# Optimization experiments

Hardware: AMD Instinct MI355X
Metric: run time of the kernel (lower is better)

The kernel has to match this reference:

```python
import jax, jax.numpy as jnp
import numpy as np
from math import sqrt


def setup_inputs() -> dict:
    key = jax.random.key(0)
    kq, kk, kv = jax.random.split(key, 3)
    B, L, H, E = 4, 2048, 8, 64
    S, D = L, E
    return {
        "queries": jax.random.normal(kq, (B, L, H, E), dtype=jnp.float32),
        "keys": jax.random.normal(kk, (B, S, H, E), dtype=jnp.float32),
        "values": jax.random.normal(kv, (B, S, H, D), dtype=jnp.float32),
    }


def reference(queries, keys, values):
    # FullAttention with mask_flag=True (TriangularCausalMask), dropout p=0,
    # output_attention=False. scale = 1/sqrt(E).
    B, L, H, E = queries.shape
    S = keys.shape[1]
    scale = 1.0 / sqrt(E)
    # scores: [B, H, L, S]
    scores = jnp.einsum("blhe,bshe->bhls", queries, keys)
    # causal mask: positions s > l are masked (upper triangle above diagonal)
    causal = jnp.tril(jnp.ones((L, S), dtype=bool))  # True = keep
    neg_inf = jnp.finfo(scores.dtype).min
    scores = jnp.where(causal, scores, neg_inf)
    A = jax.nn.softmax(scale * scores, axis=-1)  # [B,H,L,S]
    # context: [B, L, H, D]
    V = jnp.einsum("bhls,bshd->blhd", A, values)
    return V
```

## Files before the change

### kernel.cpp

```cpp
#include <hip/hip_runtime.h>
#include <math.h>

#define BD 4
#define LD 2048
#define HD 8
#define ED 64
#define TQ 128
#define TK 64
#define RS (HD * ED)

typedef __attribute__((ext_vector_type(8))) _Float16 f16x8;
typedef __attribute__((ext_vector_type(4))) _Float16 f16x4;
typedef __attribute__((ext_vector_type(4))) float f32x4;
typedef __attribute__((ext_vector_type(4))) unsigned int u32x4;
typedef __attribute__((ext_vector_type(2))) unsigned int u32x2;
typedef unsigned int u32;
typedef unsigned long long u64;

__device__ inline u32 pkh(float a, float b) {
    return __builtin_bit_cast(u32, __builtin_amdgcn_cvt_pkrtz(a, b));
}
__device__ inline u64 pkh4(float a, float b, float c, float d) {
    return (u64)pkh(a, b) | ((u64)pkh(c, d) << 32);
}
__device__ inline int swz(int row, int bcol) {
    return row * 128 + ((((bcol >> 4) ^ row) & 7) << 4) + (bcol & 15);
}

__global__ __launch_bounds__(512, 2)
void fa_mfma_kpar(const float* __restrict__ Q, const float* __restrict__ K,
                  const float* __restrict__ V, float* __restrict__ O) {
    __shared__ __align__(16) char smem[65536];

    const int t    = threadIdx.x;
    const int lane = t & 63;
    const int w    = t >> 6;
    const int wr   = w & 3;
    const int p    = w >> 2;
    const int m16  = lane & 15;
    const int quad = lane >> 4;

    const int b = blockIdx.x >> 3;
    const int h = blockIdx.x & 7;
    const int y  = (int)blockIdx.y;
    const int qt = (y < 8) ? (15 - y) : (y - 8);
    const int q0 = qt * TQ;
    const int nIter = qt + 1;

    const int tt  = t & 255;
    const int ks  = tt >> 2;
    const int ke0 = (tt & 3) << 2;
    const int vs0 = (tt & 15) << 2;
    const int vd0 = (tt >> 4) << 2;

    const float* Kbase = K + ((size_t)((b * LD + p * TK + ks) * HD + h)) * ED + ke0;
    const float* Vbase = V + ((size_t)((b * LD + p * TK + vs0) * HD + h)) * ED + vd0;

    char* const myK = smem + p * 16384;
    char* const myV = smem + 32768 + p * 16384;

    const float qscale = 0.125f * 1.44269504088896340736f;
    f16x8 qf[2][2];
    #pragma unroll
    for (int sub = 0; sub < 2; ++sub) {
        const float* qrow =
            Q + ((size_t)((b * LD + q0 + (wr << 5) + (sub << 4) + m16) * HD + h)) * ED;
        #pragma unroll
        for (int hf = 0; hf < 2; ++hf) {
            const float4 x  = *(const float4*)(qrow + hf * 32 + quad * 8);
            const float4 y4 = *(const float4*)(qrow + hf * 32 + quad * 8 + 4);
            u32x4 pk;
            pk[0] = pkh(x.x * qscale, x.y * qscale);
            pk[1] = pkh(x.z * qscale, x.w * qscale);
            pk[2] = pkh(y4.x * qscale, y4.y * qscale);
            pk[3] = pkh(y4.z * qscale, y4.w * qscale);
            qf[sub][hf] = __builtin_bit_cast(f16x8, pk);
        }
    }

    f32x4 oacc[2][4];
    float l_i[2] = {0.0f, 0.0f};
    #pragma unroll
    for (int sub = 0; sub < 2; ++sub)
        #pragma unroll
        for (int nt = 0; nt < 4; ++nt) oacc[sub][nt] = (f32x4){0.f, 0.f, 0.f, 0.f};

    float4 kx[4], vx[4];
    {
        #pragma unroll
        for (int j = 0; j < 4; ++j) kx[j] = *(const float4*)(Kbase + 16 * j);
        #pragma unroll
        for (int rr = 0; rr < 4; ++rr) vx[rr] = *(const float4*)(Vbase + rr * RS);
        #pragma unroll
        for (int j = 0; j < 4; ++j)
            *(u64*)(myK + swz(ks, 2 * (ke0 + 16 * j))) = pkh4(kx[j].x, kx[j].y, kx[j].z, kx[j].w);
        *(u64*)(myV + swz(vd0 + 0, 2 * vs0)) = pkh4(vx[0].x, vx[1].x, vx[2].x, vx[3].x);
        *(u64*)(myV + swz(vd0 + 1, 2 * vs0)) = pkh4(vx[0].y, vx[1].y, vx[2].y, vx[3].y);
        *(u64*)(myV + swz(vd0 + 2, 2 * vs0)) = pkh4(vx[0].z, vx[1].z, vx[2].z, vx[3].z);
        *(u64*)(myV + swz(vd0 + 3, 2 * vs0)) = pkh4(vx[0].w, vx[1].w, vx[2].w, vx[3].w);
    }
    __syncthreads();

    for (int it = 0; it < nIter; ++it) {
        const int kt = 2 * it + p;
        char* rK = myK + ((it & 1) << 13);
        char* rV = myV + ((it & 1) << 13);
        const bool pre = it < qt;

        if (pre) {
            const float* kp = Kbase + (size_t)(it + 1) * (2 * TK * RS);
            const float* vp = Vbase + (size_t)(it + 1) * (2 * TK * RS);
            #pragma unroll
            for (int j = 0; j < 4; ++j) kx[j] = *(const float4*)(kp + 16 * j);
            #pragma unroll
            for (int rr = 0; rr < 4; ++rr) vx[rr] = *(const float4*)(vp + rr * RS);
        }

        const int offq = (2 * qt - kt) * 64;
        if (offq + (wr << 5) + 31 >= 0) {
            f32x4 sacc[2][4];
            __builtin_amdgcn_s_setprio(1);
            #pragma unroll
            for (int kc = 0; kc < 4; ++kc) {
                const f16x8 kf0 = *(const f16x8*)(rK + swz(kc * 16 + m16, quad * 16));
                const f16x8 kf1 = *(const f16x8*)(rK + swz(kc * 16 + m16, 64 + quad * 16));
                #pragma unroll
                for (int sub = 0; sub < 2; ++sub) {
                    f32x4 z = {0.f, 0.f, 0.f, 0.f};
                    z = __builtin_amdgcn_mfma_f32_16x16x32_f16(kf0, qf[sub][0], z, 0, 0, 0);
                    z = __builtin_amdgcn_mfma_f32_16x16x32_f16(kf1, qf[sub][1], z, 0, 0, 0);
                    sacc[sub][kc] = z;
                }
            }
            __builtin_amdgcn_s_setprio(0);

            if (offq < 64) {
                #pragma unroll
                for (int sub = 0; sub < 2; ++sub) {
                    const int ql = (wr << 5) + (sub << 4) + m16 + offq;
                    #pragma unroll
                    for (int kc = 0; kc < 4; ++kc)
                        #pragma unroll
                        for (int i = 0; i < 4; ++i)
                            if (kc * 16 + quad * 4 + i > ql) sacc[sub][kc][i] = -INFINITY;
                }
            }

            f16x4 pf[2][4];
            #pragma unroll
            for (int sub = 0; sub < 2; ++sub) {
                #pragma unroll
                for (int kc = 0; kc < 4; ++kc) {
                    float p0 = __builtin_amdgcn_exp2f(sacc[sub][kc][0]);
                    float p1 = __builtin_amdgcn_exp2f(sacc[sub][kc][1]);
                    float p2 = __builtin_amdgcn_exp2f(sacc[sub][kc][2]);
                    float p3 = __builtin_amdgcn_exp2f(sacc[sub][kc][3]);
                    l_i[sub] += (p0 + p1) + (p2 + p3);
                    u32x2 pp;
                    pp[0] = pkh(p0, p1);
                    pp[1] = pkh(p2, p3);
                    pf[sub][kc] = __builtin_bit_cast(f16x4, pp);
                }
            }

            __builtin_amdgcn_s_setprio(1);
            #pragma unroll
            for (int kc = 0; kc < 4; ++kc) {
                #pragma unroll
                for (int dt = 0; dt < 4; ++dt) {
                    const f16x4 vf = *(const f16x4*)
                        (rV + swz(dt * 16 + m16, 2 * (kc * 16 + quad * 4)));
                    oacc[0][dt] = __builtin_amdgcn_mfma_f32_16x16x16f16(vf, pf[0][kc], oacc[0][dt], 0, 0, 0);
                    oacc[1][dt] = __builtin_amdgcn_mfma_f32_16x16x16f16(vf, pf[1][kc], oacc[1][dt], 0, 0, 0);
                }
            }
            __builtin_amdgcn_s_setprio(0);
        }

        if (pre) {
            char* wK = myK + ((it & 1) ? 0 : 8192);
            char* wV = myV + ((it & 1) ? 0 : 8192);
            #pragma unroll
            for (int j = 0; j < 4; ++j)
                *(u64*)(wK + swz(ks, 2 * (ke0 + 16 * j))) = pkh4(kx[j].x, kx[j].y, kx[j].z, kx[j].w);
            *(u64*)(wV + swz(vd0 + 0, 2 * vs0)) = pkh4(vx[0].x, vx[1].x, vx[2].x, vx[3].x);
            *(u64*)(wV + swz(vd0 + 1, 2 * vs0)) = pkh4(vx[0].y, vx[1].y, vx[2].y, vx[3].y);
            *(u64*)(wV + swz(vd0 + 2, 2 * vs0)) = pkh4(vx[0].z, vx[1].z, vx[2].z, vx[3].z);
            *(u64*)(wV + swz(vd0 + 3, 2 * vs0)) = pkh4(vx[0].w, vx[1].w, vx[2].w, vx[3].w);
        }
        __syncthreads();
    }

    {
        char* eo  = smem;
        float* el = (float*)(smem + 32768);
        const int erow = (wr << 6) + lane;
        if (p == 1) {
            #pragma unroll
            for (int sub = 0; sub < 2; ++sub) {
                el[erow * 2 + sub] = l_i[sub];
                #pragma unroll
                for (int dt = 0; dt < 4; ++dt)
                    *(f32x4*)(eo + swz(erow, 16 * ((sub << 2) + dt))) = oacc[sub][dt];
            }
        }
        __syncthreads();
        if (p == 0) {
            #pragma unroll
            for (int sub = 0; sub < 2; ++sub) {
                l_i[sub] += el[erow * 2 + sub];
                #pragma unroll
                for (int dt = 0; dt < 4; ++dt)
                    oacc[sub][dt] += *(const f32x4*)(eo + swz(erow, 16 * ((sub << 2) + dt)));

                float l = l_i[sub];
                l += __shfl_xor(l, 16);
                l += __shfl_xor(l, 32);
                const float inv = 1.0f / l;
                float* orow =
                    O + ((size_t)((b * LD + q0 + (wr << 5) + (sub << 4) + m16) * HD + h)) * ED;
                #pragma unroll
                for (int dt = 0; dt < 4; ++dt) {
                    float4 o;
                    o.x = oacc[sub][dt][0] * inv;
                    o.y = oacc[sub][dt][1] * inv;
                    o.z = oacc[sub][dt][2] * inv;
                    o.w = oacc[sub][dt][3] * inv;
                    *(float4*)(orow + dt * 16 + quad * 4) = o;
                }
            }
        }
    }
}

extern "C" void kernel_launch(void* const* d_in, const int* in_sizes, int n_in,
                              void* d_out, int out_size, void* d_ws, size_t ws_size,
                              hipStream_t stream) {
    const float* Q = (const float*)d_in[0];
    const float* K = (const float*)d_in[1];
    const float* V = (const float*)d_in[2];
    float* O = (float*)d_out;
    dim3 grid(BD * HD, 16);
    fa_mfma_kpar<<<grid, 512, 0, stream>>>(Q, K, V, O);
}
```

Before: 130.4 us.

## Deepen K/V global prefetch to two tiles ahead with ping-pong registers

Global loads for K/V tiles are now issued two iterations ahead, using two register buffers that alternate via a manually unrolled loop. Each step stores into LDS the tile loaded in the previous step. Clamped indices remove the branch on the prefetch and store, at the cost of redundant loads and LDS writes near the end. The aim is to hide global memory latency better, in exchange for doubling the staging registers, which may pressure occupancy at launch bounds 512,2.

```diff
diff --git a/kernel.cpp b/kernel.cpp
--- a/kernel.cpp
+++ b/kernel.cpp
@@ -25,6 +25,99 @@
 }
 __device__ inline int swz(int row, int bcol) {
     return row * 128 + ((((bcol >> 4) ^ row) & 7) << 4) + (bcol & 15);
+}
+
+__device__ __forceinline__ void fa_step(
+    int it, int qt, int p, int wr, int m16, int quad,
+    int ks, int ke0, int vs0, int vd0,
+    const float* Kbase, const float* Vbase,
+    char* myK, char* myV,
+    const f16x8 (&qf)[2][2], f32x4 (&oacc)[2][4], float (&l_i)[2],
+    float4 (&kS)[4], float4 (&vS)[4],
+    float4 (&kL)[4], float4 (&vL)[4])
+{
+    const int mm = (it + 2 <= qt) ? (it + 2) : qt;
+    const float* kp = Kbase + (size_t)mm * (2 * TK * RS);
+    const float* vp = Vbase + (size_t)mm * (2 * TK * RS);
+    #pragma unroll
+    for (int j = 0; j < 4; ++j) kL[j] = *(const float4*)(kp + 16 * j);
+    #pragma unroll
+    for (int rr = 0; rr < 4; ++rr) vL[rr] = *(const float4*)(vp + rr * RS);
+
+    char* rK = myK + ((it & 1) << 13);
+    char* rV = myV + ((it & 1) << 13);
+    const int kt = 2 * it + p;
+    const int offq = (2 * qt - kt) * 64;
+    if (offq + (wr << 5) + 31 >= 0) {
+        f32x4 sacc[2][4];
+        __builtin_amdgcn_s_setprio(1);
+        #pragma unroll
+        for (int kc = 0; kc < 4; ++kc) {
+            const f16x8 kf0 = *(const f16x8*)(rK + swz(kc * 16 + m16, quad * 16));
+            const f16x8 kf1 = *(const f16x8*)(rK + swz(kc * 16 + m16, 64 + quad * 16));
+            #pragma unroll
+            for (int sub = 0; sub < 2; ++sub) {
+                f32x4 z = {0.f, 0.f, 0.f, 0.f};
+                z = __builtin_amdgcn_mfma_f32_16x16x32_f16(kf0, qf[sub][0], z, 0, 0, 0);
+                z = __builtin_amdgcn_mfma_f32_16x16x32_f16(kf1, qf[sub][1], z, 0, 0, 0);
+                sacc[sub][kc] = z;
+            }
+        }
+        __builtin_amdgcn_s_setprio(0);
+
+        if (offq < 64) {
+            #pragma unroll
+            for (int sub = 0; sub < 2; ++sub) {
+                const int ql = (wr << 5) + (sub << 4) + m16 + offq;
+                #pragma unroll
+                for (int kc = 0; kc < 4; ++kc)
+                    #pragma unroll
+                    for (int i = 0; i < 4; ++i)
+                        if (kc * 16 + quad * 4 + i > ql) sacc[sub][kc][i] = -INFINITY;
+            }
+        }
+
+        f16x4 pf[2][4];
+        #pragma unroll
+        for (int sub = 0; sub < 2; ++sub) {
+            #pragma unroll
+            for (int kc = 0; kc < 4; ++kc) {
+                float p0 = __builtin_amdgcn_exp2f(sacc[sub][kc][0]);
+                float p1 = __builtin_amdgcn_exp2f(sacc[sub][kc][1]);
+                float p2 = __builtin_amdgcn_exp2f(sacc[sub][kc][2]);
+                float p3 = __builtin_amdgcn_exp2f(sacc[sub][kc][3]);
+                l_i[sub] += (p0 + p1) + (p2 + p3);
+                u32x2 pp;
+                pp[0] = pkh(p0, p1);
+                pp[1] = pkh(p2, p3);
+                pf[sub][kc] = __builtin_bit_cast(f16x4, pp);
+            }
+        }
+
+        __builtin_amdgcn_s_setprio(1);
+        #pragma unroll
+        for (int kc = 0; kc < 4; ++kc) {
+            #pragma unroll
+            for (int dt = 0; dt < 4; ++dt) {
+                const f16x4 vf = *(const f16x4*)
+                    (rV + swz(dt * 16 + m16, 2 * (kc * 16 + quad * 4)));
+                oacc[0][dt] = __builtin_amdgcn_mfma_f32_16x16x16f16(vf, pf[0][kc], oacc[0][dt], 0, 0, 0);
+                oacc[1][dt] = __builtin_amdgcn_mfma_f32_16x16x16f16(vf, pf[1][kc], oacc[1][dt], 0, 0, 0);
+            }
+        }
+        __builtin_amdgcn_s_setprio(0);
+    }
+
+    char* wK = myK + (((it & 1) ^ 1) << 13);
+    char* wV = myV + (((it & 1) ^ 1) << 13);
+    #pragma unroll
+    for (int j = 0; j < 4; ++j)
+        *(u64*)(wK + swz(ks, 2 * (ke0 + 16 * j))) = pkh4(kS[j].x, kS[j].y, kS[j].z, kS[j].w);
+    *(u64*)(wV + swz(vd0 + 0, 2 * vs0)) = pkh4(vS[0].x, vS[1].x, vS[2].x, vS[3].x);
+    *(u64*)(wV + swz(vd0 + 1, 2 * vs0)) = pkh4(vS[0].y, vS[1].y, vS[2].y, vS[3].y);
+    *(u64*)(wV + swz(vd0 + 2, 2 * vs0)) = pkh4(vS[0].z, vS[1].z, vS[2].z, vS[3].z);
+    *(u64*)(wV + swz(vd0 + 3, 2 * vs0)) = pkh4(vS[0].w, vS[1].w, vS[2].w, vS[3].w);
+    __syncthreads();
 }
 
 __global__ __launch_bounds__(512, 2)
@@ -85,111 +178,41 @@
         #pragma unroll
         for (int nt = 0; nt < 4; ++nt) oacc[sub][nt] = (f32x4){0.f, 0.f, 0.f, 0.f};
 
-    float4 kx[4], vx[4];
+    float4 kA[4], vA[4], kB[4], vB[4];
+
     {
         #pragma unroll
-        for (int j = 0; j < 4; ++j) kx[j] = *(const float4*)(Kbase + 16 * j);
-        #pragma unroll
-        for (int rr = 0; rr < 4; ++rr) vx[rr] = *(const float4*)(Vbase + rr * RS);
+        for (int j = 0; j < 4; ++j) kB[j] = *(const float4*)(Kbase + 16 * j);
+        #pragma unroll
+        for (int rr = 0; rr < 4; ++rr) vB[rr] = *(const float4*)(Vbase + rr * RS);
         #pragma unroll
         for (int j = 0; j < 4; ++j)
-            *(u64*)(myK + swz(ks, 2 * (ke0 + 16 * j))) = pkh4(kx[j].x, kx[j].y, kx[j].z, kx[j].w);
-        *(u64*)(myV + swz(vd0 + 0, 2 * vs0)) = pkh4(vx[0].x, vx[1].x, vx[2].x, vx[3].x);
-        *(u64*)(myV + swz(vd0 + 1, 2 * vs0)) = pkh4(vx[0].y, vx[1].y, vx[2].y, vx[3].y);
-        *(u64*)(myV + swz(vd0 + 2, 2 * vs0)) = pkh4(vx[0].z, vx[1].z, vx[2].z, vx[3].z);
-        *(u64*)(myV + swz(vd0 + 3, 2 * vs0)) = pkh4(vx[0].w, vx[1].w, vx[2].w, vx[3].w);
+            *(u64*)(myK + swz(ks, 2 * (ke0 + 16 * j))) = pkh4(kB[j].x, kB[j].y, kB[j].z, kB[j].w);
+        *(u64*)(myV + swz(vd0 + 0, 2 * vs0)) = pkh4(vB[0].x, vB[1].x, vB[2].x, vB[3].x);
+        *(u64*)(myV + swz(vd0 + 1, 2 * vs0)) = pkh4(vB[0].y, vB[1].y, vB[2].y, vB[3].y);
+        *(u64*)(myV + swz(vd0 + 2, 2 * vs0)) = pkh4(vB[0].z, vB[1].z, vB[2].z, vB[3].z);
+        *(u64*)(myV + swz(vd0 + 3, 2 * vs0)) = pkh4(vB[0].w, vB[1].w, vB[2].w, vB[3].w);
+
+        const int mm = (1 <= qt) ? 1 : qt;
+        const float* kp = Kbase + (size_t)mm * (2 * TK * RS);
+        const float* vp = Vbase + (size_t)mm * (2 * TK * RS);
+        #pragma unroll
+        for (int j = 0; j < 4; ++j) kA[j] = *(const float4*)(kp + 16 * j);
+        #pragma unroll
+        for (int rr = 0; rr < 4; ++rr) vA[rr] = *(const float4*)(vp + rr * RS);
     }
     __syncthreads();
 
-    for (int it = 0; it < nIter; ++it) {
-        const int kt = 2 * it + p;
-        char* rK = myK + ((it & 1) << 13);
-        char* rV = myV + ((it & 1) << 13);
-        const bool pre = it < qt;
-
-        if (pre) {
-            const float* kp = Kbase + (size_t)(it + 1) * (2 * TK * RS);
-            const float* vp = Vbase + (size_t)(it + 1) * (2 * TK * RS);
-            #pragma unroll
-            for (int j = 0; j < 4; ++j) kx[j] = *(const float4*)(kp + 16 * j);
-            #pragma unroll
-            for (int rr = 0; rr < 4; ++rr) vx[rr] = *(const float4*)(vp + rr * RS);
-        }
-
-        const int offq = (2 * qt - kt) * 64;
-        if (offq + (wr << 5) + 31 >= 0) {
-            f32x4 sacc[2][4];
-            __builtin_amdgcn_s_setprio(1);
-            #pragma unroll
-            for (int kc = 0; kc < 4; ++kc) {
-                const f16x8 kf0 = *(const f16x8*)(rK + swz(kc * 16 + m16, quad * 16));
-                const f16x8 kf1 = *(const f16x8*)(rK + swz(kc * 16 + m16, 64 + quad * 16));
-                #pragma unroll
-                for (int sub = 0; sub < 2; ++sub) {
-                    f32x4 z = {0.f, 0.f, 0.f, 0.f};
-                    z = __builtin_amdgcn_mfma_f32_16x16x32_f16(kf0, qf[sub][0], z, 0, 0, 0);
-                    z = __builtin_amdgcn_mfma_f32_16x16x32_f16(kf1, qf[sub][1], z, 0, 0, 0);
-                    sacc[sub][kc] = z;
-                }
-            }
-            __builtin_amdgcn_s_setprio(0);
-
-            if (offq < 64) {
-                #pragma unroll
-                for (int sub = 0; sub < 2; ++sub) {
-                    const int ql = (wr << 5) + (sub << 4) + m16 + offq;
-                    #pragma unroll
-                    for (int kc = 0; kc < 4; ++kc)
-                        #pragma unroll
-                        for (int i = 0; i < 4; ++i)
-                            if (kc * 16 + quad * 4 + i > ql) sacc[sub][kc][i] = -INFINITY;
-                }
-            }
-
-            f16x4 pf[2][4];
-            #pragma unroll
-            for (int sub = 0; sub < 2; ++sub) {
-                #pragma unroll
-                for (int kc = 0; kc < 4; ++kc) {
-                    float p0 = __builtin_amdgcn_exp2f(sacc[sub][kc][0]);
-                    float p1 = __builtin_amdgcn_exp2f(sacc[sub][kc][1]);
-                    float p2 = __builtin_amdgcn_exp2f(sacc[sub][kc][2]);
-                    float p3 = __builtin_amdgcn_exp2f(sacc[sub][kc][3]);
-                    l_i[sub] += (p0 + p1) + (p2 + p3);
-                    u32x2 pp;
-                    pp[0] = pkh(p0, p1);
-                    pp[1] = pkh(p2, p3);
-                    pf[sub][kc] = __builtin_bit_cast(f16x4, pp);
-                }
-            }
-
-            __builtin_amdgcn_s_setprio(1);
-            #pragma unroll
-            for (int kc = 0; kc < 4; ++kc) {
-                #pragma unroll
-                for (int dt = 0; dt < 4; ++dt) {
-                    const f16x4 vf = *(const f16x4*)
-                        (rV + swz(dt * 16 + m16, 2 * (kc * 16 + quad * 4)));
-                    oacc[0][dt] = __builtin_amdgcn_mfma_f32_16x16x16f16(vf, pf[0][kc], oacc[0][dt], 0, 0, 0);
-                    oacc[1][dt] = __builtin_amdgcn_mfma_f32_16x16x16f16(vf, pf[1][kc], oacc[1][dt], 0, 0, 0);
-                }
-            }
-            __builtin_amdgcn_s_setprio(0);
-        }
-
-        if (pre) {
-            char* wK = myK + ((it & 1) ? 0 : 8192);
-            char* wV = myV + ((it & 1) ? 0 : 8192);
-            #pragma unroll
-            for (int j = 0; j < 4; ++j)
-                *(u64*)(wK + swz(ks, 2 * (ke0 + 16 * j))) = pkh4(kx[j].x, kx[j].y, kx[j].z, kx[j].w);
-            *(u64*)(wV + swz(vd0 + 0, 2 * vs0)) = pkh4(vx[0].x, vx[1].x, vx[2].x, vx[3].x);
-            *(u64*)(wV + swz(vd0 + 1, 2 * vs0)) = pkh4(vx[0].y, vx[1].y, vx[2].y, vx[3].y);
-            *(u64*)(wV + swz(vd0 + 2, 2 * vs0)) = pkh4(vx[0].z, vx[1].z, vx[2].z, vx[3].z);
-            *(u64*)(wV + swz(vd0 + 3, 2 * vs0)) = pkh4(vx[0].w, vx[1].w, vx[2].w, vx[3].w);
-        }
-        __syncthreads();
-    }
+    int it = 0;
+    for (; it + 1 < nIter; it += 2) {
+        fa_step(it,     qt, p, wr, m16, quad, ks, ke0, vs0, vd0,
+                Kbase, Vbase, myK, myV, qf, oacc, l_i, kA, vA, kB, vB);
+        fa_step(it + 1, qt, p, wr, m16, quad, ks, ke0, vs0, vd0,
+                Kbase, Vbase, myK, myV, qf, oacc, l_i, kB, vB, kA, vA);
+    }
+    if (it < nIter)
+        fa_step(it,     qt, p, wr, m16, quad, ks, ke0, vs0, vd0,
+                Kbase, Vbase, myK, myV, qf, oacc, l_i, kA, vA, kB, vB);
 
     {
         char* eo  = smem;
```

New measurement: 132.3 us. Within noise of the previous version (+1.5%).
